# Kernel optimization log

Measured on AMD Instinct MI355X. Metric: run time of the kernel, lower is better.

Reference implementation:

```python
import jax, jax.numpy as jnp
import numpy as np

N = 8192
F_IN = 256
F_OUT = 128
SLOPE = 0.2
NEG_INF = -9000000000000000.0


def setup_inputs() -> dict:
    key = jax.random.key(0)
    k1, k2, k3, k4, k5 = jax.random.split(key, 5)
    x = jax.random.normal(k1, (N, F_IN), dtype=jnp.float32)
    adj = jax.random.randint(k2, (N, N), 0, 2).astype(jnp.float32)
    W = jax.random.normal(k3, (F_IN, F_OUT), dtype=jnp.float32) * (1.0 / np.sqrt(F_IN))
    a_src = jax.random.normal(k4, (F_OUT,), dtype=jnp.float32) * (1.0 / np.sqrt(F_OUT))
    a_dst = jax.random.normal(k5, (F_OUT,), dtype=jnp.float32) * (1.0 / np.sqrt(F_OUT))
    return {"x": x, "adj": adj, "W": W, "a_src": a_src, "a_dst": a_dst}


def reference(x, adj, W, a_src, a_dst):
    # h: (N, F_OUT)
    h = x @ W
    f_src = h @ a_src  # (N,)
    f_dst = h @ a_dst  # (N,)
    # additive attention scores: (N, N)
    e = f_src[:, None] + f_dst[None, :]
    e = jnp.where(e >= 0, e, SLOPE * e)  # leaky_relu
    e = jnp.where(adj > 0, e, NEG_INF)
    alpha = jax.nn.softmax(e, axis=1)  # (N, N)
    return alpha @ h  # (N, F_OUT)
```

## Files before the change

kernel.cpp:

```cpp
#include <hip/hip_runtime.h>
#include <hip/hip_bf16.h>

#define NN 8192
#define FIN 256
#define FO 128
#define KSPLIT 16
#define JCHUNK 512
#define NSTEP 8
#define SGN 2
#define MSTRIDE 10
#define L2E 1.4426950408889634f
#define C2  0.28853900817779268f

typedef __bf16 bf16x8 __attribute__((ext_vector_type(8)));
typedef __bf16 bf16x2 __attribute__((ext_vector_type(2)));
typedef float  f32x4  __attribute__((ext_vector_type(4)));
typedef unsigned long long u64;
typedef u64 u64x2 __attribute__((ext_vector_type(2)));

__global__ __launch_bounds__(256) void k_proj(
    const float* __restrict__ x, const float* __restrict__ W,
    const float* __restrict__ a_src, const float* __restrict__ a_dst,
    __bf16* __restrict__ Bp, float* __restrict__ f_src, float* __restrict__ f_dst)
{
  __shared__ float xs[16 * FIN];
  __shared__ float fs[16], fd[16];
  const int tid = threadIdx.x;
  const int i0 = blockIdx.x * 16;

  const float4* xg = (const float4*)(x + (size_t)i0 * FIN);
  float4* xs4 = (float4*)xs;
  #pragma unroll
  for (int t = 0; t < 4; t++) xs4[tid + 256 * t] = xg[tid + 256 * t];
  if (tid < 16) { fs[tid] = 0.f; fd[tid] = 0.f; }
  __syncthreads();

  const int cq = tid & 31;
  const int rg = tid >> 5;
  const int c0 = cq * 4;
  const int r0 = rg * 2;
  float acc0[4] = {0.f,0.f,0.f,0.f};
  float acc1[4] = {0.f,0.f,0.f,0.f};
  const float* xr0 = xs + r0 * FIN;
  const float* xr1 = xs + (r0 + 1) * FIN;

  for (int k = 0; k < FIN; k += 4) {
    float4 xa = *(const float4*)(xr0 + k);
    float4 xb = *(const float4*)(xr1 + k);
    #pragma unroll
    for (int kk = 0; kk < 4; kk++) {
      float4 wv = *(const float4*)(W + (size_t)(k + kk) * FO + c0);
      float xav = ((const float*)&xa)[kk];
      float xbv = ((const float*)&xb)[kk];
      acc0[0] += xav * wv.x; acc0[1] += xav * wv.y;
      acc0[2] += xav * wv.z; acc0[3] += xav * wv.w;
      acc1[0] += xbv * wv.x; acc1[1] += xbv * wv.y;
      acc1[2] += xbv * wv.z; acc1[3] += xbv * wv.w;
    }
  }

  float4 as = *(const float4*)(a_src + c0);
  float4 ad = *(const float4*)(a_dst + c0);
  float ps0 = acc0[0]*as.x + acc0[1]*as.y + acc0[2]*as.z + acc0[3]*as.w;
  float ps1 = acc1[0]*as.x + acc1[1]*as.y + acc1[2]*as.z + acc1[3]*as.w;
  float pd0 = acc0[0]*ad.x + acc0[1]*ad.y + acc0[2]*ad.z + acc0[3]*ad.w;
  float pd1 = acc1[0]*ad.x + acc1[1]*ad.y + acc1[2]*ad.z + acc1[3]*ad.w;
  atomicAdd(&fs[r0],     ps0);
  atomicAdd(&fs[r0 + 1], ps1);
  atomicAdd(&fd[r0],     pd0);
  atomicAdd(&fd[r0 + 1], pd1);

  const int j0 = i0 + r0;
  const int kg = j0 >> 5;
  const int q  = (j0 >> 3) & 3;
  const int t0 = j0 & 7;
  #pragma unroll
  for (int c = 0; c < 4; c++) {
    const int n = c0 + c;
    bf16x2 v;
    v[0] = (__bf16)acc0[c];
    v[1] = (__bf16)acc1[c];
    size_t idx = ((size_t)(kg * 8 + (n >> 4)) * 64 + q * 16 + (n & 15)) * 8 + t0;
    *(bf16x2*)(Bp + idx) = v;
  }
  __syncthreads();
  if (tid < 16) { f_src[i0 + tid] = fs[tid]; f_dst[i0 + tid] = fd[tid]; }
}

__global__ __launch_bounds__(256) void k_attn(
    const float* __restrict__ adj, const __bf16* __restrict__ Bp,
    const float* __restrict__ f_src, const float* __restrict__ f_dst,
    float* __restrict__ part, float* __restrict__ lpart)
{
  __shared__ float G1[JCHUNK];
  __shared__ float G2[JCHUNK];
  __shared__ __align__(16) u64 msk[128][MSTRIDE];

  const int tid = threadIdx.x;
  const int rb = blockIdx.x >> 4;
  const int ks = blockIdx.x & 15;
  const int i0 = rb * 128;
  const int jbase = ks * JCHUNK;

  const int w = tid >> 6;
  const int lane = tid & 63;
  const int m = lane & 15;
  const int q = lane >> 4;
  const int wbase = i0 + w * 32;

  float F1[2], F2[2];
  #pragma unroll
  for (int mt = 0; mt < 2; mt++) {
    float s = f_src[wbase + mt * 16 + m];
    F1[mt] = __builtin_amdgcn_exp2f(s * L2E);
    F2[mt] = __builtin_amdgcn_exp2f(s * C2);
  }

  #pragma unroll
  for (int t = 0; t < 2; t++) {
    int j = tid + t * 256;
    float d = f_dst[jbase + j];
    G1[j] = __builtin_amdgcn_exp2f(d * L2E);
    G2[j] = __builtin_amdgcn_exp2f(d * C2);
  }
  __syncthreads();

  const float* abase = adj + (size_t)wbase * NN + jbase + lane * 4;
  #pragma unroll 2
  for (int rr = 0; rr < 32; ++rr) {
    const float* rp = abase + (size_t)rr * NN;
    float4 c0 = *(const float4*)rp;
    float4 c1 = *(const float4*)(rp + 256);
    u64 w00 = __ballot(c0.x > 0.f);
    u64 w01 = __ballot(c0.y > 0.f);
    u64 w02 = __ballot(c0.z > 0.f);
    u64 w03 = __ballot(c0.w > 0.f);
    u64 w10 = __ballot(c1.x > 0.f);
    u64 w11 = __ballot(c1.y > 0.f);
    u64 w12 = __ballot(c1.z > 0.f);
    u64 w13 = __ballot(c1.w > 0.f);
    if (lane < 8) {
      u64 v = lane == 0 ? w00 : lane == 1 ? w01 : lane == 2 ? w02 :
              lane == 3 ? w03 : lane == 4 ? w10 : lane == 5 ? w11 :
              lane == 6 ? w12 : w13;
      msk[w * 32 + rr][lane] = v;
    }
  }

  f32x4 acc[2][8];
  #pragma unroll
  for (int mt = 0; mt < 2; mt++)
    #pragma unroll
    for (int nt = 0; nt < 8; nt++) acc[mt][nt] = (f32x4){0.f, 0.f, 0.f, 0.f};
  float psum[2] = {0.f, 0.f};

  const int r0l = w * 32 + m;
  const __bf16* bsrc_base = Bp + (size_t)ks * 16 * 4096 + lane * 8;

  for (int sg = 0; sg < SGN; ++sg) {
    u64x2 Ma01 = *(const u64x2*)&msk[r0l][sg * 4];
    u64x2 Ma23 = *(const u64x2*)&msk[r0l][sg * 4 + 2];
    u64x2 Mb01 = *(const u64x2*)&msk[r0l + 16][sg * 4];
    u64x2 Mb23 = *(const u64x2*)&msk[r0l + 16][sg * 4 + 2];

    #pragma unroll
    for (int ss = 0; ss < 4; ++ss) {
      const int step = sg * 4 + ss;
      #pragma unroll
      for (int kg = 0; kg < 2; kg++) {
        const int jj = step * 64 + kg * 32 + q * 8;
        float4 u0 = *(const float4*)(G1 + jj);
        float4 u1 = *(const float4*)(G1 + jj + 4);
        float4 v0 = *(const float4*)(G2 + jj);
        float4 v1 = *(const float4*)(G2 + jj + 4);
        const unsigned b = ss * 16 + kg * 8 + q * 2;

        bf16x8 af[2];
        #pragma unroll
        for (int mt = 0; mt < 2; mt++) {
          const u64 M0 = mt ? Mb01[0] : Ma01[0];
          const u64 M1 = mt ? Mb01[1] : Ma01[1];
          const u64 M2 = mt ? Mb23[0] : Ma23[0];
          const u64 M3 = mt ? Mb23[1] : Ma23[1];
          const unsigned e0 = (unsigned)(M0 >> b);
          const unsigned e1 = (unsigned)(M1 >> b);
          const unsigned e2 = (unsigned)(M2 >> b);
          const unsigned e3 = (unsigned)(M3 >> b);
          const float f1 = F1[mt], f2 = F2[mt];
          float p0 = (e0 & 1u) ? fmaxf(f1 * u0.x, f2 * v0.x) : 0.f;
          float p1 = (e1 & 1u) ? fmaxf(f1 * u0.y, f2 * v0.y) : 0.f;
          float p2 = (e2 & 1u) ? fmaxf(f1 * u0.z, f2 * v0.z) : 0.f;
          float p3 = (e3 & 1u) ? fmaxf(f1 * u0.w, f2 * v0.w) : 0.f;
          float p4 = (e0 & 2u) ? fmaxf(f1 * u1.x, f2 * v1.x) : 0.f;
          float p5 = (e1 & 2u) ? fmaxf(f1 * u1.y, f2 * v1.y) : 0.f;
          float p6 = (e2 & 2u) ? fmaxf(f1 * u1.z, f2 * v1.z) : 0.f;
          float p7 = (e3 & 2u) ? fmaxf(f1 * u1.w, f2 * v1.w) : 0.f;
          psum[mt] += ((p0 + p1) + (p2 + p3)) + ((p4 + p5) + (p6 + p7));
          bf16x8 a;
          a[0] = (__bf16)p0; a[1] = (__bf16)p1; a[2] = (__bf16)p2;
          a[3] = (__bf16)p3; a[4] = (__bf16)p4; a[5] = (__bf16)p5;
          a[6] = (__bf16)p6; a[7] = (__bf16)p7;
          af[mt] = a;
        }

        const __bf16* bsrc = bsrc_base + (size_t)(step * 2 + kg) * 4096;
        #pragma unroll
        for (int nt = 0; nt < 8; nt++) {
          bf16x8 bfrag = *(const bf16x8*)(bsrc + nt * 512);
          acc[0][nt] = __builtin_amdgcn_mfma_f32_16x16x32_bf16(af[0], bfrag, acc[0][nt], 0, 0, 0);
          acc[1][nt] = __builtin_amdgcn_mfma_f32_16x16x32_bf16(af[1], bfrag, acc[1][nt], 0, 0, 0);
        }
      }
    }
  }

  float* ldst = lpart + (size_t)ks * NN;
  #pragma unroll
  for (int mt = 0; mt < 2; mt++) {
    float p = psum[mt];
    p += __shfl_xor(p, 16);
    p += __shfl_xor(p, 32);
    if (lane < 16) ldst[wbase + mt * 16 + lane] = p;
  }

  float* pdst = part + (size_t)ks * NN * FO;
  #pragma unroll
  for (int mt = 0; mt < 2; mt++) {
    const int rb0 = wbase + mt * 16 + q * 4;
    #pragma unroll
    for (int nt = 0; nt < 8; nt++) {
      #pragma unroll
      for (int r = 0; r < 4; r++) {
        pdst[(size_t)(rb0 + r) * FO + nt * 16 + m] = acc[mt][nt][r];
      }
    }
  }
}

__global__ __launch_bounds__(256) void k_div(
    const float* __restrict__ part, const float* __restrict__ lpart,
    float* __restrict__ out)
{
  int idx = blockIdx.x * 256 + threadIdx.x;
  int row = idx >> 5;
  float4 s = {0.f, 0.f, 0.f, 0.f};
  float l = 0.f;
  #pragma unroll
  for (int ks = 0; ks < KSPLIT; ks++) {
    float4 v = ((const float4*)(part + (size_t)ks * NN * FO))[idx];
    s.x += v.x; s.y += v.y; s.z += v.z; s.w += v.w;
    l += lpart[ks * NN + row];
  }
  float inv = 1.0f / l;
  float4 o;
  o.x = s.x * inv; o.y = s.y * inv; o.z = s.z * inv; o.w = s.w * inv;
  ((float4*)out)[idx] = o;
}

extern "C" void kernel_launch(void* const* d_in, const int* in_sizes, int n_in,
                              void* d_out, int out_size, void* d_ws, size_t ws_size,
                              hipStream_t stream) {
  const float* x     = (const float*)d_in[0];
  const float* adj   = (const float*)d_in[1];
  const float* W     = (const float*)d_in[2];
  const float* a_src = (const float*)d_in[3];
  const float* a_dst = (const float*)d_in[4];
  float* out = (float*)d_out;

  char* ws = (char*)d_ws;
  __bf16* Bp   = (__bf16*)ws;
  float* f_src = (float*)(ws + 2097152);
  float* f_dst = (float*)(ws + 2097152 + 32768);
  float* part  = (float*)(ws + 16777216);
  float* lpart = (float*)(ws + 83886080);

  hipLaunchKernelGGL(k_proj, dim3(512), dim3(256), 0, stream,
                     x, W, a_src, a_dst, Bp, f_src, f_dst);
  hipLaunchKernelGGL(k_attn, dim3(1024), dim3(256), 0, stream,
                     adj, Bp, f_src, f_dst, part, lpart);
  hipLaunchKernelGGL(k_div, dim3(1024), dim3(256), 0, stream,
                     part, lpart, out);
}
```

Baseline: 468.2 us.

## Split attention output columns across wave pairs and double the block count

Each k_attn block now covers 64 rows instead of 128. Pairs of waves share the same 32 rows and each wave computes half of the 128 output columns. This halves the accumulator registers and allows a launch-bounds occupancy hint of 4 blocks per CU, with twice as many blocks launched. In exchange, the exp/mask probability computation is done twice per row pair, and the adjacency mask load is spread across waves before the barrier.

```diff
diff --git a/kernel.cpp b/kernel.cpp
--- a/kernel.cpp
+++ b/kernel.cpp
@@ -87,26 +87,28 @@
   if (tid < 16) { f_src[i0 + tid] = fs[tid]; f_dst[i0 + tid] = fd[tid]; }
 }
 
-__global__ __launch_bounds__(256) void k_attn(
+__global__ __launch_bounds__(256, 4) void k_attn(
     const float* __restrict__ adj, const __bf16* __restrict__ Bp,
     const float* __restrict__ f_src, const float* __restrict__ f_dst,
     float* __restrict__ part, float* __restrict__ lpart)
 {
   __shared__ float G1[JCHUNK];
   __shared__ float G2[JCHUNK];
-  __shared__ __align__(16) u64 msk[128][MSTRIDE];
+  __shared__ __align__(16) u64 msk[64][MSTRIDE];
 
   const int tid = threadIdx.x;
   const int rb = blockIdx.x >> 4;
   const int ks = blockIdx.x & 15;
-  const int i0 = rb * 128;
+  const int i0 = rb * 64;
   const int jbase = ks * JCHUNK;
 
   const int w = tid >> 6;
   const int lane = tid & 63;
   const int m = lane & 15;
   const int q = lane >> 4;
-  const int wbase = i0 + w * 32;
+  const int p  = w >> 1;
+  const int nh = w & 1;
+  const int wbase = i0 + p * 32;
 
   float F1[2], F2[2];
   #pragma unroll
@@ -123,39 +125,42 @@
     G1[j] = __builtin_amdgcn_exp2f(d * L2E);
     G2[j] = __builtin_amdgcn_exp2f(d * C2);
   }
+
+  {
+    const int prow = p * 32 + nh * 16;
+    const float* abase = adj + (size_t)(i0 + prow) * NN + jbase + lane * 4;
+    #pragma unroll 2
+    for (int rr = 0; rr < 16; ++rr) {
+      const float* rp = abase + (size_t)rr * NN;
+      float4 c0 = *(const float4*)rp;
+      float4 c1 = *(const float4*)(rp + 256);
+      u64 w00 = __ballot(c0.x > 0.f);
+      u64 w01 = __ballot(c0.y > 0.f);
+      u64 w02 = __ballot(c0.z > 0.f);
+      u64 w03 = __ballot(c0.w > 0.f);
+      u64 w10 = __ballot(c1.x > 0.f);
+      u64 w11 = __ballot(c1.y > 0.f);
+      u64 w12 = __ballot(c1.z > 0.f);
+      u64 w13 = __ballot(c1.w > 0.f);
+      if (lane < 8) {
+        u64 v = lane == 0 ? w00 : lane == 1 ? w01 : lane == 2 ? w02 :
+                lane == 3 ? w03 : lane == 4 ? w10 : lane == 5 ? w11 :
+                lane == 6 ? w12 : w13;
+        msk[prow + rr][lane] = v;
+      }
+    }
+  }
   __syncthreads();
 
-  const float* abase = adj + (size_t)wbase * NN + jbase + lane * 4;
-  #pragma unroll 2
-  for (int rr = 0; rr < 32; ++rr) {
-    const float* rp = abase + (size_t)rr * NN;
-    float4 c0 = *(const float4*)rp;
-    float4 c1 = *(const float4*)(rp + 256);
-    u64 w00 = __ballot(c0.x > 0.f);
-    u64 w01 = __ballot(c0.y > 0.f);
-    u64 w02 = __ballot(c0.z > 0.f);
-    u64 w03 = __ballot(c0.w > 0.f);
-    u64 w10 = __ballot(c1.x > 0.f);
-    u64 w11 = __ballot(c1.y > 0.f);
-    u64 w12 = __ballot(c1.z > 0.f);
-    u64 w13 = __ballot(c1.w > 0.f);
-    if (lane < 8) {
-      u64 v = lane == 0 ? w00 : lane == 1 ? w01 : lane == 2 ? w02 :
-              lane == 3 ? w03 : lane == 4 ? w10 : lane == 5 ? w11 :
-              lane == 6 ? w12 : w13;
-      msk[w * 32 + rr][lane] = v;
-    }
-  }
-
-  f32x4 acc[2][8];
+  f32x4 acc[2][4];
   #pragma unroll
   for (int mt = 0; mt < 2; mt++)
     #pragma unroll
-    for (int nt = 0; nt < 8; nt++) acc[mt][nt] = (f32x4){0.f, 0.f, 0.f, 0.f};
+    for (int nt = 0; nt < 4; nt++) acc[mt][nt] = (f32x4){0.f, 0.f, 0.f, 0.f};
   float psum[2] = {0.f, 0.f};
 
-  const int r0l = w * 32 + m;
-  const __bf16* bsrc_base = Bp + (size_t)ks * 16 * 4096 + lane * 8;
+  const int r0l = p * 32 + m;
+  const __bf16* bsrc_base = Bp + (size_t)ks * 16 * 4096 + (size_t)nh * 4 * 512 + lane * 8;
 
   for (int sg = 0; sg < SGN; ++sg) {
     u64x2 Ma01 = *(const u64x2*)&msk[r0l][sg * 4];
@@ -195,7 +200,8 @@
           float p5 = (e1 & 2u) ? fmaxf(f1 * u1.y, f2 * v1.y) : 0.f;
           float p6 = (e2 & 2u) ? fmaxf(f1 * u1.z, f2 * v1.z) : 0.f;
           float p7 = (e3 & 2u) ? fmaxf(f1 * u1.w, f2 * v1.w) : 0.f;
-          psum[mt] += ((p0 + p1) + (p2 + p3)) + ((p4 + p5) + (p6 + p7));
+          if (nh == 0)
+            psum[mt] += ((p0 + p1) + (p2 + p3)) + ((p4 + p5) + (p6 + p7));
           bf16x8 a;
           a[0] = (__bf16)p0; a[1] = (__bf16)p1; a[2] = (__bf16)p2;
           a[3] = (__bf16)p3; a[4] = (__bf16)p4; a[5] = (__bf16)p5;
@@ -205,7 +211,7 @@
 
         const __bf16* bsrc = bsrc_base + (size_t)(step * 2 + kg) * 4096;
         #pragma unroll
-        for (int nt = 0; nt < 8; nt++) {
+        for (int nt = 0; nt < 4; nt++) {
           bf16x8 bfrag = *(const bf16x8*)(bsrc + nt * 512);
           acc[0][nt] = __builtin_amdgcn_mfma_f32_16x16x32_bf16(af[0], bfrag, acc[0][nt], 0, 0, 0);
           acc[1][nt] = __builtin_amdgcn_mfma_f32_16x16x32_bf16(af[1], bfrag, acc[1][nt], 0, 0, 0);
@@ -214,13 +220,15 @@
     }
   }
 
-  float* ldst = lpart + (size_t)ks * NN;
-  #pragma unroll
-  for (int mt = 0; mt < 2; mt++) {
-    float p = psum[mt];
-    p += __shfl_xor(p, 16);
-    p += __shfl_xor(p, 32);
-    if (lane < 16) ldst[wbase + mt * 16 + lane] = p;
+  if (nh == 0) {
+    float* ldst = lpart + (size_t)ks * NN;
+    #pragma unroll
+    for (int mt = 0; mt < 2; mt++) {
+      float pp = psum[mt];
+      pp += __shfl_xor(pp, 16);
+      pp += __shfl_xor(pp, 32);
+      if (lane < 16) ldst[wbase + mt * 16 + lane] = pp;
+    }
   }
 
   float* pdst = part + (size_t)ks * NN * FO;
@@ -228,10 +236,10 @@
   for (int mt = 0; mt < 2; mt++) {
     const int rb0 = wbase + mt * 16 + q * 4;
     #pragma unroll
-    for (int nt = 0; nt < 8; nt++) {
+    for (int nt = 0; nt < 4; nt++) {
       #pragma unroll
       for (int r = 0; r < 4; r++) {
-        pdst[(size_t)(rb0 + r) * FO + nt * 16 + m] = acc[mt][nt][r];
+        pdst[(size_t)(rb0 + r) * FO + (nh * 4 + nt) * 16 + m] = acc[mt][nt][r];
       }
     }
   }
@@ -276,7 +284,7 @@
 
   hipLaunchKernelGGL(k_proj, dim3(512), dim3(256), 0, stream,
                      x, W, a_src, a_dst, Bp, f_src, f_dst);
-  hipLaunchKernelGGL(k_attn, dim3(1024), dim3(256), 0, stream,
+  hipLaunchKernelGGL(k_attn, dim3(2048), dim3(256), 0, stream,
                      adj, Bp, f_src, f_dst, part, lpart);
   hipLaunchKernelGGL(k_div, dim3(1024), dim3(256), 0, stream,
                      part, lpart, out);
```

New measurement: 447.4 us. 1.05x faster.
